# Optimization experiments

Measured on AMD Instinct MI355X. Metric: run time of the kernel, lower is better.

## Reference

```python
import jax, jax.numpy as jnp
import numpy as np

B, S, D, L = 4, 4096, 2048, 4
QH, KVH, WINDOW = 16, 4, 512
HD = D // QH
G = QH // KVH
CAPF = 0.25
EPS = float(jnp.finfo(jnp.float32).eps)  # torch RMSNorm default eps for fp32


def setup_inputs() -> dict:
    key = jax.random.key(0)
    ks = jax.random.split(key, 8)
    s = 0.02
    return {
        "x": jax.random.normal(ks[0], (B, S, D), jnp.float32),
        "router_w": jax.random.normal(ks[1], (1, D), jnp.float32) * s,
        "norm1_w": jnp.ones((L, D), jnp.float32),
        "norm2_w": jnp.ones((L, D), jnp.float32),
        "qkv_w": jax.random.normal(ks[2], (L, (QH + 2 * KVH) * HD, D), jnp.float32) * s,
        "proj_w": jax.random.normal(ks[3], (L, D, D), jnp.float32) * s,
        "fc1_w": jax.random.normal(ks[4], (L, 2 * D, D), jnp.float32) * s,
        "fc2_w": jax.random.normal(ks[5], (L, D, D), jnp.float32) * s,
    }


def rmsnorm(x, w):
    return x * jax.lax.rsqrt(jnp.mean(x * x, -1, keepdims=True) + EPS) * w


def gqa(x, qkv_w, proj_w):
    # x: [B, C, D]; causal sliding-window attention with ALiBi (flash_attn semantics)
    b, c, _ = x.shape
    qkv = x @ qkv_w.T
    q = qkv[..., : QH * HD].reshape(b, c, KVH, G, HD)
    k = qkv[..., QH * HD:(QH + KVH) * HD].reshape(b, c, KVH, HD)
    v = qkv[..., (QH + KVH) * HD:].reshape(b, c, KVH, HD)
    scale = 1.0 / np.sqrt(HD)
    scores = jnp.einsum('bqkgd,bskd->bkgqs', q, k) * scale  # [B,KVH,G,C,C]
    i = jnp.arange(c)[:, None]
    j = jnp.arange(c)[None, :]
    diff = (i - j).astype(jnp.float32)
    mask = (diff >= 0) & (diff <= WINDOW)  # causal + left window
    slopes = jnp.exp2(-((jnp.arange(QH, dtype=jnp.float32) + 1.0) * 8.0 / QH))
    slopes = slopes.reshape(KVH, G, 1, 1)  # q head h = kvh*G + g ordering
    scores = jnp.where(mask, scores - slopes * diff, -jnp.inf)
    p = jax.nn.softmax(scores, axis=-1)
    att = jnp.einsum('bkgqs,bskd->bqkgd', p, v).reshape(b, c, QH * HD)
    return att @ proj_w.T


def swiglu(x, fc1_w, fc2_w):
    h = x @ fc1_w.T
    a, gate = jnp.split(h, 2, axis=-1)
    return (jax.nn.silu(gate) * a) @ fc2_w.T


def reference(x, router_w, norm1_w, norm2_w, qkv_w, proj_w, fc1_w, fc2_w):
    b, s, d = x.shape
    rw = jax.nn.sigmoid(x @ router_w.T)  # [B, S, 1]
    cap = int(s * CAPF)  # training path: capacity = int(seq_len * capacity_factor)
    rws = rw[..., 0]
    _, top_idx = jax.lax.top_k(rws, cap)            # unsorted-by-position top-k
    idx_sorted = jnp.sort(top_idx, axis=1)          # restore sequence order
    order = jnp.argsort(top_idx, axis=1)
    # faithful to source: gathers router_weights at the sort-order permutation
    # indices (values in [0, cap)), exactly as torch.gather(router_weights, 1, router_top_order)
    top_w = jnp.take_along_axis(rws, order, axis=1)[..., None]  # [B, cap, 1]
    lat = jnp.take_along_axis(x, idx_sorted[..., None], axis=1)  # [B, cap, D]
    for l in range(L):
        lat = lat + gqa(rmsnorm(lat, norm1_w[l]), qkv_w[l], proj_w[l])
        lat = lat + swiglu(rmsnorm(lat, norm2_w[l]), fc1_w[l], fc2_w[l])
    lat = lat * top_w
    bidx = jnp.arange(b)[:, None]
    pred = jnp.zeros_like(x).at[bidx, idx_sorted].set(lat)
    decisions = jnp.zeros_like(rw).at[bidx, idx_sorted].set(1.0)
    return pred, rw, decisions
```

## Files before the change

### kernel.cpp

```cpp
#include <hip/hip_runtime.h>
#include <hip/hip_bf16.h>

constexpr int NB = 4;
constexpr int SEQ = 4096;
constexpr int DIM = 2048;
constexpr int NLAYER = 4;
constexpr int NQH = 16;
constexpr int NKVH = 4;
constexpr int WIN = 512;
constexpr int HDIM = 128;
constexpr int CAPN = 1024;
constexpr int MTOK = NB * CAPN;
constexpr int QKVN = (NQH + 2 * NKVH) * HDIM;
constexpr int VOFF = DIM + NKVH * HDIM;
constexpr float EPSF = 1.1920928955078125e-07f;

typedef __hip_bfloat16 bf16;
typedef __bf16 b16x8 __attribute__((ext_vector_type(8)));
typedef __bf16 b16x4 __attribute__((ext_vector_type(4)));
typedef float f32x4 __attribute__((ext_vector_type(4)));

#define MFMA16(a, b, c) __builtin_amdgcn_mfma_f32_16x16x32_bf16((a), (b), (c), 0, 0, 0)

__device__ __forceinline__ void gload_lds16(const void* g, void* l) {
  __builtin_amdgcn_global_load_lds((__attribute__((address_space(1))) void*)(void*)g,
                                   (__attribute__((address_space(3))) void*)l, 16, 0, 0);
}

__global__ __launch_bounds__(256) void cast_kernel(const float* __restrict__ in,
                                                   bf16* __restrict__ out, int n) {
  int i = (blockIdx.x * 256 + threadIdx.x) * 4;
  if (i >= n) return;
  float4 v = *(const float4*)(in + i);
  b16x4 o;
  o[0] = (__bf16)v.x; o[1] = (__bf16)v.y; o[2] = (__bf16)v.z; o[3] = (__bf16)v.w;
  *(b16x4*)((__bf16*)out + i) = o;
}

__global__ __launch_bounds__(256) void router_kernel(const float* __restrict__ x,
                                                     const float* __restrict__ rwt,
                                                     float* __restrict__ rw_out) {
  int tok = blockIdx.x * 4 + (threadIdx.x >> 6);
  int l = threadIdx.x & 63;
  const float* xr = x + (size_t)tok * DIM;
  float s = 0.f;
  for (int c = l; c < DIM; c += 64) s += xr[c] * rwt[c];
  for (int off = 32; off; off >>= 1) s += __shfl_down(s, off);
  if (l == 0) rw_out[tok] = 1.f / (1.f + expf(-s));
}

__global__ __launch_bounds__(256) void rankcnt_kernel(const float* __restrict__ rw,
                                                      int* __restrict__ rank) {
  int blk = blockIdx.x;
  int ic = blk & 15, jc = (blk >> 4) & 15, b = blk >> 8;
  __shared__ float4 svi[64];
  int t = threadIdx.x;
  if (t < 64) svi[t] = ((const float4*)(rw + (size_t)b * SEQ + ic * 256))[t];
  __syncthreads();
  int j = jc * 256 + t;
  float vj = rw[(size_t)b * SEQ + j];
  int r = 0;
#pragma unroll 16
  for (int q = 0; q < 64; ++q) {
    float4 v = svi[q];
    int i = ic * 256 + q * 4;
    r += (v.x > vj || (v.x == vj && (i + 0) < j)) ? 1 : 0;
    r += (v.y > vj || (v.y == vj && (i + 1) < j)) ? 1 : 0;
    r += (v.z > vj || (v.z == vj && (i + 2) < j)) ? 1 : 0;
    r += (v.w > vj || (v.w == vj && (i + 3) < j)) ? 1 : 0;
  }
  atomicAdd(&rank[b * SEQ + j], r);
}

__global__ __launch_bounds__(1024) void select_kernel(const int* __restrict__ rank,
                                                      const float* __restrict__ rw,
                                                      int* __restrict__ idxs,
                                                      float* __restrict__ topw,
                                                      float* __restrict__ dec) {
  int b = blockIdx.x;
  int t = threadIdx.x;
  __shared__ int sr[SEQ];
  __shared__ int scnt[1024];
  for (int i = t; i < SEQ; i += 1024) sr[i] = rank[b * SEQ + i];
  __syncthreads();
  for (int i = t; i < SEQ; i += 1024) dec[(size_t)b * SEQ + i] = (sr[i] < CAPN) ? 1.0f : 0.0f;
  int c = 0;
#pragma unroll
  for (int k = 0; k < 4; ++k) c += (sr[t * 4 + k] < CAPN) ? 1 : 0;
  scnt[t] = c;
  __syncthreads();
  for (int off = 1; off < 1024; off <<= 1) {
    int v = scnt[t];
    int vm = (t >= off) ? scnt[t - off] : 0;
    __syncthreads();
    scnt[t] = v + vm;
    __syncthreads();
  }
  int pos = scnt[t] - c;
  for (int k = 0; k < 4; ++k) {
    int j = t * 4 + k;
    int r = sr[j];
    if (r < CAPN) {
      idxs[b * CAPN + pos] = j;
      topw[b * CAPN + pos] = rw[(size_t)b * SEQ + r];
      pos++;
    }
  }
}

__global__ __launch_bounds__(256) void gather_kernel(const float* __restrict__ x,
                                                     const int* __restrict__ idxs,
                                                     float* __restrict__ lat) {
  int tok = blockIdx.x;
  int b = tok >> 10, i = tok & 1023;
  int src = idxs[b * CAPN + i];
  const float4* sp = (const float4*)(x + ((size_t)b * SEQ + src) * DIM);
  float4* dp = (float4*)(lat + (size_t)tok * DIM);
  int t = threadIdx.x;
  dp[t] = sp[t];
  dp[t + 256] = sp[t + 256];
}

__global__ __launch_bounds__(256) void rmsnorm_kernel(const float* __restrict__ in,
                                                      const float* __restrict__ w,
                                                      bf16* __restrict__ out) {
  int row = blockIdx.x;
  int t = threadIdx.x;
  const float4* sp = (const float4*)(in + (size_t)row * DIM);
  float4 v0 = sp[t], v1 = sp[t + 256];
  float ss = v0.x * v0.x + v0.y * v0.y + v0.z * v0.z + v0.w * v0.w +
             v1.x * v1.x + v1.y * v1.y + v1.z * v1.z + v1.w * v1.w;
  for (int off = 32; off; off >>= 1) ss += __shfl_down(ss, off);
  __shared__ float red[4];
  if ((t & 63) == 0) red[t >> 6] = ss;
  __syncthreads();
  float total = red[0] + red[1] + red[2] + red[3];
  float sc = rsqrtf(total * (1.0f / DIM) + EPSF);
  const float4* wp = (const float4*)w;
  float4 w0 = wp[t], w1 = wp[t + 256];
  __bf16* op = (__bf16*)out + (size_t)row * DIM;
  b16x4 o0, o1;
  o0[0] = (__bf16)(v0.x * w0.x * sc); o0[1] = (__bf16)(v0.y * w0.y * sc);
  o0[2] = (__bf16)(v0.z * w0.z * sc); o0[3] = (__bf16)(v0.w * w0.w * sc);
  o1[0] = (__bf16)(v1.x * w1.x * sc); o1[1] = (__bf16)(v1.y * w1.y * sc);
  o1[2] = (__bf16)(v1.z * w1.z * sc); o1[3] = (__bf16)(v1.w * w1.w * sc);
  *(b16x4*)(op + t * 4) = o0;
  *(b16x4*)(op + 1024 + t * 4) = o1;
}


__device__ __forceinline__ void stage_half(const bf16* g, int K, int kt,
                                           bf16* tilebase, int h, int tid) {
#pragma unroll
  for (int j = 0; j < 2; ++j) {
    int q = h * 16384 + j * 8192 + tid * 16;
    int row = q >> 7;
    int sc = ((tid & 7) ^ (row & 7)) << 3;
    gload_lds16((const __bf16*)g + (size_t)row * K + kt * 64 + sc,
                (char*)tilebase + q);
  }
}

__device__ __forceinline__ b16x8 frag8(const bf16* buf, int row, int ks, int hi) {
  int co = (ks * 32 + hi * 8) ^ ((row & 7) << 3);
  return *(const b16x8*)((const __bf16*)buf + row * 64 + co);
}

template <bool VT>
__global__ __launch_bounds__(512) void gemm8p(const bf16* __restrict__ A,
                                              const bf16* __restrict__ Bw,
                                              bf16* __restrict__ Cb,
                                              bf16* __restrict__ vTout,
                                              int N, int K, int nbn) {
  __shared__ __align__(16) bf16 sA[2][256 * 64];
  __shared__ __align__(16) bf16 sB[2][256 * 64];
  const int tid = threadIdx.x;
  const int w = tid >> 6, l = tid & 63;
  const int lo = l & 15, hi = l >> 4;
  const int wm = w >> 2, wn = w & 3;
  const int nwg = gridDim.x;
  int bid = blockIdx.x;
  bid = (bid & 7) * (nwg >> 3) + (bid >> 3);
  const int bm = bid / nbn, bn = bid % nbn;
  const bf16* Ab = A + (size_t)bm * 256 * K;
  const bf16* Bb = Bw + (size_t)bn * 256 * K;
  const int nt = K >> 6;
  const int niter = nt >> 1;

  f32x4 acc[8][4];
#pragma unroll
  for (int i = 0; i < 8; ++i)
#pragma unroll
    for (int j = 0; j < 4; ++j) acc[i][j] = f32x4{0.f, 0.f, 0.f, 0.f};

#define LDA_Q(BUF, QM)                                                      \
  do {                                                                      \
    _Pragma("unroll") for (int mi = 0; mi < 4; ++mi)                        \
        _Pragma("unroll") for (int ks = 0; ks < 2; ++ks)                    \
            af[mi][ks] = frag8((BUF), wm * 128 + (QM)*64 + mi * 16 + lo, ks, hi); \
  } while (0)
#define LDB_Q(BUF, QN, DST)                                                 \
  do {                                                                      \
    _Pragma("unroll") for (int ni = 0; ni < 2; ++ni)                        \
        _Pragma("unroll") for (int ks = 0; ks < 2; ++ks)                    \
            DST[ni][ks] = frag8((BUF), wn * 64 + (QN)*32 + ni * 16 + lo, ks, hi); \
  } while (0)
#define MM_Q(QM, QN, BFR)                                                   \
  do {                                                                      \
    __builtin_amdgcn_s_setprio(1);                                          \
    _Pragma("unroll") for (int ks = 0; ks < 2; ++ks)                        \
        _Pragma("unroll") for (int mi = 0; mi < 4; ++mi)                    \
            _Pragma("unroll") for (int ni = 0; ni < 2; ++ni)                \
                acc[(QM)*4 + mi][(QN)*2 + ni] =                             \
                    MFMA16(af[mi][ks], BFR[ni][ks], acc[(QM)*4 + mi][(QN)*2 + ni]); \
    __builtin_amdgcn_s_setprio(0);                                          \
  } while (0)
#define BAR() __builtin_amdgcn_s_barrier()

  stage_half(Ab, K, 0, sA[0], 0, tid);
  stage_half(Ab, K, 0, sA[0], 1, tid);
  stage_half(Bb, K, 0, sB[0], 0, tid);
  stage_half(Bb, K, 0, sB[0], 1, tid);
  stage_half(Bb, K, 1, sB[1], 0, tid);
  stage_half(Bb, K, 1, sB[1], 1, tid);
  stage_half(Ab, K, 1, sA[1], 0, tid);
  asm volatile("s_waitcnt vmcnt(6)" ::: "memory");
  __builtin_amdgcn_sched_barrier(0);
  BAR();

  for (int i = 0; i < niter; ++i) {
    const int t0 = 2 * i;
    const bool s2 = (t0 + 2) < nt;
    b16x8 af[4][2], bf0[2][2], bf1[2][2];
    LDA_Q(sA[0], 0); LDB_Q(sB[0], 0, bf0);
    stage_half(Ab, K, t0 + 1, sA[1], 1, tid);
    BAR(); MM_Q(0, 0, bf0); BAR();
    LDB_Q(sB[0], 1, bf1);
    BAR(); MM_Q(0, 1, bf1); BAR();
    LDA_Q(sA[0], 1);
    if (s2) stage_half(Bb, K, t0 + 2, sB[0], 0, tid);
    BAR(); MM_Q(1, 0, bf0); BAR();
    if (s2) stage_half(Bb, K, t0 + 2, sB[0], 1, tid);
    BAR(); MM_Q(1, 1, bf1);
    if (s2) asm volatile("s_waitcnt vmcnt(4)" ::: "memory");
    else    asm volatile("s_waitcnt vmcnt(0)" ::: "memory");
    __builtin_amdgcn_sched_barrier(0);
    BAR();
    LDA_Q(sA[1], 0); LDB_Q(sB[1], 0, bf0);
    if (s2) stage_half(Ab, K, t0 + 2, sA[0], 0, tid);
    BAR(); MM_Q(0, 0, bf0); BAR();
    LDB_Q(sB[1], 1, bf1);
    if (s2) stage_half(Ab, K, t0 + 2, sA[0], 1, tid);
    BAR(); MM_Q(0, 1, bf1); BAR();
    LDA_Q(sA[1], 1);
    if (s2) { stage_half(Bb, K, t0 + 3, sB[1], 0, tid);
              stage_half(Bb, K, t0 + 3, sB[1], 1, tid); }
    BAR(); MM_Q(1, 0, bf0); BAR();
    if (s2) stage_half(Ab, K, t0 + 3, sA[1], 0, tid);
    BAR(); MM_Q(1, 1, bf1);
    if (s2) {
      asm volatile("s_waitcnt vmcnt(6)" ::: "memory");
      __builtin_amdgcn_sched_barrier(0);
    }
    BAR();
  }
#undef LDA_Q
#undef LDB_Q
#undef MM_Q
#undef BAR

#pragma unroll
  for (int fi = 0; fi < 8; ++fi) {
    int row0 = bm * 256 + wm * 128 + fi * 16 + hi * 4;
#pragma unroll
    for (int fj = 0; fj < 4; ++fj) {
      int col = bn * 256 + wn * 64 + fj * 16 + lo;
#pragma unroll
      for (int r = 0; r < 4; ++r) {
        bf16 bv = __float2bfloat16(acc[fi][fj][r]);
        Cb[(size_t)(row0 + r) * N + col] = bv;
        if constexpr (VT) {
          if (col >= VOFF) {
            int cc = col - VOFF;
            int kvh = cc >> 7, d = cc & 127;
            int row = row0 + r;
            int bb = row >> 10, tk = row & 1023;
            vTout[((size_t)(bb * NKVH + kvh) * HDIM + d) * CAPN + tk] = bv;
          }
        }
      }
    }
  }
}

template <int ROWS>
__device__ __forceinline__ void stage_tile(const bf16* gbase, int ldk, int kt,
                                           bf16* lbuf, int tid) {
#pragma unroll
  for (int i = 0; i < ROWS / 128; ++i) {
    int q = i * 8192 + tid * 16;
    int row = q >> 6;
    int ce = ((tid & 3) ^ ((row >> 1) & 3)) << 3;
    gload_lds16((const __bf16*)gbase + (size_t)row * ldk + kt * 32 + ce,
                (char*)lbuf + q);
  }
}

__device__ __forceinline__ b16x8 frag_ld(const bf16* buf, int row, int hi) {
  int ce = (hi ^ ((row >> 1) & 3)) << 3;
  return *(const b16x8*)((const __bf16*)buf + row * 32 + ce);
}

template <int MR, bool ADD, bool OUTBF>
__global__ __launch_bounds__(512, 2) void gemm256(const bf16* __restrict__ A,
                                                  const bf16* __restrict__ Bw,
                                                  float* __restrict__ Cf,
                                                  bf16* __restrict__ Cb,
                                                  bf16* __restrict__ vTout,
                                                  int N, int K, int nbn) {
  constexpr int BM = MR * 32;
  constexpr int PH = MR / 4;
  __shared__ __align__(16) bf16 sA[4][BM * 32];
  __shared__ __align__(16) bf16 sB[4][256 * 32];
  const int tid = threadIdx.x;
  const int w = tid >> 6, l = tid & 63;
  const int lo = l & 15, hi = l >> 4;
  const int wm = w >> 2, wn = w & 3;
  const int nwg = gridDim.x;
  int bid = blockIdx.x;
  bid = (bid & 7) * (nwg >> 3) + (bid >> 3);
  const int bm = bid / nbn, bn = bid % nbn;
  const bf16* Ab = A + (size_t)bm * BM * K;
  const bf16* Bb = Bw + (size_t)bn * 256 * K;
  const int nt = K >> 5;

  f32x4 acc[MR][4];
#pragma unroll
  for (int i = 0; i < MR; ++i)
#pragma unroll
    for (int j = 0; j < 4; ++j) acc[i][j] = f32x4{0.f, 0.f, 0.f, 0.f};

  for (int tt = 0; tt < 3; ++tt) {
    stage_tile<BM>(Ab, K, tt, sA[tt], tid);
    stage_tile<256>(Bb, K, tt, sB[tt], tid);
  }
  if constexpr (MR == 8) asm volatile("s_waitcnt vmcnt(8)" ::: "memory");
  else                   asm volatile("s_waitcnt vmcnt(6)" ::: "memory");
  __builtin_amdgcn_sched_barrier(0);
  __builtin_amdgcn_s_barrier();

  for (int t = 0; t < nt; ++t) {
    const bf16* bufA = sA[t & 3];
    const bf16* bufB = sB[t & 3];
    b16x8 bfr[4];
#pragma unroll
    for (int p = 0; p < PH; ++p) {
      b16x8 af[4];
#pragma unroll
      for (int mi = 0; mi < 4; ++mi)
        af[mi] = frag_ld(bufA, wm * (MR * 16) + p * 64 + mi * 16 + lo, hi);
      if (p == 0) {
#pragma unroll
        for (int ni = 0; ni < 4; ++ni)
          bfr[ni] = frag_ld(bufB, wn * 64 + ni * 16 + lo, hi);
      }
      if (t + 3 < nt) {
        if (p == 0) stage_tile<BM>(Ab, K, t + 3, sA[(t + 3) & 3], tid);
        if (p == PH - 1) stage_tile<256>(Bb, K, t + 3, sB[(t + 3) & 3], tid);
      }
      __builtin_amdgcn_s_barrier();
      __builtin_amdgcn_s_setprio(1);
#pragma unroll
      for (int mi = 0; mi < 4; ++mi)
#pragma unroll
        for (int ni = 0; ni < 4; ++ni)
          acc[p * 4 + mi][ni] = MFMA16(af[mi], bfr[ni], acc[p * 4 + mi][ni]);
      __builtin_amdgcn_s_setprio(0);
      if (p == PH - 1) {
        if (t + 3 < nt) {
          if constexpr (MR == 8) asm volatile("s_waitcnt vmcnt(8)" ::: "memory");
          else                   asm volatile("s_waitcnt vmcnt(6)" ::: "memory");
        } else if (t + 2 < nt) {
          if constexpr (MR == 8) asm volatile("s_waitcnt vmcnt(4)" ::: "memory");
          else                   asm volatile("s_waitcnt vmcnt(3)" ::: "memory");
        } else if (t + 1 < nt) {
          asm volatile("s_waitcnt vmcnt(0)" ::: "memory");
        }
        __builtin_amdgcn_sched_barrier(0);
      }
      __builtin_amdgcn_s_barrier();
    }
  }

#pragma unroll
  for (int mi = 0; mi < MR; ++mi) {
    int row0 = bm * BM + wm * (MR * 16) + mi * 16 + hi * 4;
#pragma unroll
    for (int ni = 0; ni < 4; ++ni) {
      int col = bn * 256 + wn * 64 + ni * 16 + lo;
#pragma unroll
      for (int r = 0; r < 4; ++r) {
        size_t idx = (size_t)(row0 + r) * N + col;
        float v = acc[mi][ni][r];
        if constexpr (ADD) v += Cf[idx];
        if constexpr (OUTBF) {
          Cb[idx] = __float2bfloat16(v);
        } else {
          Cf[idx] = v;
        }
      }
    }
  }
}

__global__ __launch_bounds__(256) void attn_kernel(const bf16* __restrict__ qkvb,
                                                   const bf16* __restrict__ vT,
                                                   bf16* __restrict__ attb) {
  const int blk = blockIdx.x;
  const int qc = blk & 31;
  const int kvh = (blk >> 5) & 3;
  const int b = blk >> 7;
  const int w = threadIdx.x >> 6, l = threadIdx.x & 63;
  const int lo = l & 15, hi = l >> 4;
  const int h = kvh * 4 + w;
  const float slope = exp2f(-0.5f * (float)(h + 1));
  const float scale = 0.08838834764831845f;
  __shared__ __align__(16) bf16 p_lds[4][2][16 * 32];
  const __bf16* qp = (const __bf16*)qkvb;
  const __bf16* vtp = (const __bf16*)vT + (size_t)(b * NKVH + kvh) * HDIM * CAPN;
  const size_t tb = (size_t)b * CAPN;
  const int i0b = qc * 32;

  b16x8 aq[2][4];
#pragma unroll
  for (int qt = 0; qt < 2; ++qt) {
    const __bf16* qrow = qp + (tb + i0b + qt * 16 + lo) * QKVN + h * HDIM + hi * 8;
#pragma unroll
    for (int c = 0; c < 4; ++c) aq[qt][c] = *(const b16x8*)(qrow + c * 32);
  }

  f32x4 acc[2][8];
#pragma unroll
  for (int qt = 0; qt < 2; ++qt)
#pragma unroll
    for (int d = 0; d < 8; ++d) acc[qt][d] = f32x4{0.f, 0.f, 0.f, 0.f};
  float mrow[2][4], ssum[2][4];
#pragma unroll
  for (int qt = 0; qt < 2; ++qt)
#pragma unroll
    for (int r = 0; r < 4; ++r) { mrow[qt][r] = -1e30f; ssum[qt][r] = 0.f; }

  int jlo = i0b - WIN;
  if (jlo < 0) jlo = 0;
  jlo &= ~31;
  for (int j0 = jlo; j0 <= i0b; j0 += 32) {
    b16x8 kf[2][4];
#pragma unroll
    for (int jt = 0; jt < 2; ++jt) {
      const __bf16* krow = qp + (tb + j0 + jt * 16 + lo) * QKVN + DIM + kvh * HDIM + hi * 8;
#pragma unroll
      for (int c = 0; c < 4; ++c) kf[jt][c] = *(const b16x8*)(krow + c * 32);
    }
    f32x4 s[2][2];
#pragma unroll
    for (int qt = 0; qt < 2; ++qt)
#pragma unroll
      for (int jt = 0; jt < 2; ++jt) {
        s[qt][jt] = f32x4{0.f, 0.f, 0.f, 0.f};
#pragma unroll
        for (int c = 0; c < 4; ++c) s[qt][jt] = MFMA16(aq[qt][c], kf[jt][c], s[qt][jt]);
      }
#pragma unroll
    for (int qt = 0; qt < 2; ++qt) {
#pragma unroll
      for (int r = 0; r < 4; ++r) {
        const int i = i0b + qt * 16 + hi * 4 + r;
        float d0f = (float)(i - (j0 + lo));
        float d1f = (float)(i - (j0 + 16 + lo));
        float v0 = (d0f >= 0.f && d0f <= 512.f) ? (s[qt][0][r] * scale - slope * d0f) : -1e30f;
        float v1 = (d1f >= 0.f && d1f <= 512.f) ? (s[qt][1][r] * scale - slope * d1f) : -1e30f;
        float tm = fmaxf(v0, v1);
#pragma unroll
        for (int off = 1; off < 16; off <<= 1) tm = fmaxf(tm, __shfl_xor(tm, off));
        float mnew = fmaxf(mrow[qt][r], tm);
        float e0 = (v0 > -1e29f) ? __expf(v0 - mnew) : 0.f;
        float e1 = (v1 > -1e29f) ? __expf(v1 - mnew) : 0.f;
        float rs = e0 + e1;
#pragma unroll
        for (int off = 1; off < 16; off <<= 1) rs += __shfl_xor(rs, off);
        float corr = (mrow[qt][r] > -1e29f) ? __expf(mrow[qt][r] - mnew) : 0.f;
        ssum[qt][r] = ssum[qt][r] * corr + rs;
        mrow[qt][r] = mnew;
#pragma unroll
        for (int d = 0; d < 8; ++d) acc[qt][d][r] *= corr;
        p_lds[w][qt][(hi * 4 + r) * 32 + lo] = __float2bfloat16(e0);
        p_lds[w][qt][(hi * 4 + r) * 32 + 16 + lo] = __float2bfloat16(e1);
      }
    }
    b16x8 pa[2];
    pa[0] = *(const b16x8*)((const __bf16*)p_lds[w][0] + lo * 32 + hi * 8);
    pa[1] = *(const b16x8*)((const __bf16*)p_lds[w][1] + lo * 32 + hi * 8);
#pragma unroll
    for (int dh = 0; dh < 2; ++dh) {
      b16x8 bv[4];
#pragma unroll
      for (int dd = 0; dd < 4; ++dd) {
        int d = dh * 4 + dd;
        bv[dd] = *(const b16x8*)(vtp + (size_t)(d * 16 + lo) * CAPN + j0 + hi * 8);
      }
#pragma unroll
      for (int qt = 0; qt < 2; ++qt)
#pragma unroll
        for (int dd = 0; dd < 4; ++dd)
          acc[qt][dh * 4 + dd] = MFMA16(pa[qt], bv[dd], acc[qt][dh * 4 + dd]);
    }
  }
#pragma unroll
  for (int qt = 0; qt < 2; ++qt)
#pragma unroll
    for (int d = 0; d < 8; ++d)
#pragma unroll
      for (int r = 0; r < 4; ++r) {
        int row = i0b + qt * 16 + hi * 4 + r;
        attb[(tb + row) * DIM + h * HDIM + d * 16 + lo] =
            __float2bfloat16(acc[qt][d][r] / ssum[qt][r]);
      }
}

__global__ __launch_bounds__(256) void swiglu_kernel(const bf16* __restrict__ hb,
                                                     bf16* __restrict__ out) {
  int row = blockIdx.x;
  int c = threadIdx.x * 8;
  const __bf16* hp = (const __bf16*)hb + (size_t)row * (2 * DIM);
  b16x8 a8 = *(const b16x8*)(hp + c);
  b16x8 g8 = *(const b16x8*)(hp + DIM + c);
  b16x8 o;
#pragma unroll
  for (int i = 0; i < 8; ++i) {
    float a = (float)a8[i], g = (float)g8[i];
    float sg = g / (1.f + __expf(-g));
    o[i] = (__bf16)(sg * a);
  }
  *(b16x8*)((__bf16*)out + (size_t)row * DIM + c) = o;
}

__global__ __launch_bounds__(256) void scatter_kernel(const float* __restrict__ lat,
                                                      const int* __restrict__ idxs,
                                                      const float* __restrict__ topw,
                                                      float* __restrict__ pred) {
  int tok = blockIdx.x;
  int b = tok >> 10, i = tok & 1023;
  int dst = idxs[b * CAPN + i];
  float wv = topw[b * CAPN + i];
  const float4* sp = (const float4*)(lat + (size_t)tok * DIM);
  float4* dp = (float4*)(pred + ((size_t)b * SEQ + dst) * DIM);
  int t = threadIdx.x;
  float4 v = sp[t];
  v.x *= wv; v.y *= wv; v.z *= wv; v.w *= wv;
  dp[t] = v;
  v = sp[t + 256];
  v.x *= wv; v.y *= wv; v.z *= wv; v.w *= wv;
  dp[t + 256] = v;
}

extern "C" void kernel_launch(void* const* d_in, const int* in_sizes, int n_in,
                              void* d_out, int out_size, void* d_ws, size_t ws_size,
                              hipStream_t stream) {
  const float* x        = (const float*)d_in[0];
  const float* router_w = (const float*)d_in[1];
  const float* norm1_w  = (const float*)d_in[2];
  const float* norm2_w  = (const float*)d_in[3];
  const float* qkv_w    = (const float*)d_in[4];
  const float* proj_w   = (const float*)d_in[5];
  const float* fc1_w    = (const float*)d_in[6];
  const float* fc2_w    = (const float*)d_in[7];

  float* pred   = (float*)d_out;
  float* rw_out = pred + (size_t)NB * SEQ * DIM;
  float* dec    = rw_out + (size_t)NB * SEQ;

  char* ws = (char*)d_ws;
  float* lat  = (float*)ws; ws += (size_t)MTOK * DIM * 4;
  bf16* xn    = (bf16*)ws;  ws += (size_t)MTOK * DIM * 2;
  bf16* qkvb  = (bf16*)ws;  ws += (size_t)MTOK * QKVN * 2;
  bf16* attb  = (bf16*)ws;  ws += (size_t)MTOK * DIM * 2;
  int* rank   = (int*)ws;   ws += (size_t)NB * SEQ * 4;
  int* idxs   = (int*)ws;   ws += (size_t)NB * CAPN * 4;
  float* topw = (float*)ws; ws += (size_t)NB * CAPN * 4;

  char* sp = (char*)pred;
  bf16* hb = (bf16*)sp; sp += (size_t)MTOK * (2 * DIM) * 2;
  bf16* wq = (bf16*)sp; sp += (size_t)QKVN * DIM * 2;
  bf16* wp = (bf16*)sp; sp += (size_t)DIM * DIM * 2;
  bf16* w1 = (bf16*)sp; sp += (size_t)(2 * DIM) * DIM * 2;
  bf16* w2 = (bf16*)sp; sp += (size_t)DIM * DIM * 2;
  bf16* vT = (bf16*)sp; sp += (size_t)NB * NKVH * HDIM * CAPN * 2;

  router_kernel<<<NB * SEQ / 4, 256, 0, stream>>>(x, router_w, rw_out);
  hipMemsetAsync(rank, 0, (size_t)NB * SEQ * 4, stream);
  rankcnt_kernel<<<NB * 256, 256, 0, stream>>>(rw_out, rank);
  select_kernel<<<NB, 1024, 0, stream>>>(rank, rw_out, idxs, topw, dec);
  gather_kernel<<<MTOK, 256, 0, stream>>>(x, idxs, lat);

  for (int l = 0; l < NLAYER; ++l) {
    cast_kernel<<<(QKVN * DIM) / 1024, 256, 0, stream>>>(qkv_w + (size_t)l * QKVN * DIM, wq, QKVN * DIM);
    cast_kernel<<<(DIM * DIM) / 1024, 256, 0, stream>>>(proj_w + (size_t)l * DIM * DIM, wp, DIM * DIM);
    cast_kernel<<<(2 * DIM * DIM) / 1024, 256, 0, stream>>>(fc1_w + (size_t)l * 2 * DIM * DIM, w1, 2 * DIM * DIM);
    cast_kernel<<<(DIM * DIM) / 1024, 256, 0, stream>>>(fc2_w + (size_t)l * DIM * DIM, w2, DIM * DIM);

    rmsnorm_kernel<<<MTOK, 256, 0, stream>>>(lat, norm1_w + (size_t)l * DIM, xn);
    gemm8p<true><<<(MTOK / 256) * (QKVN / 256), 512, 0, stream>>>(
        xn, wq, qkvb, vT, QKVN, DIM, QKVN / 256);
    attn_kernel<<<NB * NKVH * 32, 256, 0, stream>>>(qkvb, vT, attb);
    gemm256<4, true, false><<<(MTOK / 128) * (DIM / 256), 512, 0, stream>>>(
        attb, wp, lat, nullptr, nullptr, DIM, DIM, DIM / 256);

    rmsnorm_kernel<<<MTOK, 256, 0, stream>>>(lat, norm2_w + (size_t)l * DIM, xn);
    gemm8p<false><<<(MTOK / 256) * (2 * DIM / 256), 512, 0, stream>>>(
        xn, w1, hb, nullptr, 2 * DIM, DIM, 2 * DIM / 256);
    swiglu_kernel<<<MTOK, 256, 0, stream>>>(hb, xn);
    gemm256<4, true, false><<<(MTOK / 128) * (DIM / 256), 512, 0, stream>>>(
        xn, w2, lat, nullptr, nullptr, DIM, DIM, DIM / 256);
  }

  hipMemsetAsync(pred, 0, (size_t)NB * SEQ * DIM * 4, stream);
  scatter_kernel<<<MTOK, 256, 0, stream>>>(lat, idxs, topw, pred);
}
```

Measured before the change: 1.675 ms.

## Fuse SwiGLU into fc1 GEMM epilogue via interleaved fc1 weight rows

The fc1 weight cast now interleaves the 'a' and 'gate' rows in 16-row chunks, so each 16-column MFMA fragment pair in the GEMM holds matching a/gate columns. The fc1 GEMM epilogue then applies silu(gate)*a directly and writes the DIM-wide bf16 activation, which removes the separate swiglu kernel and the round trip of the 2*DIM-wide intermediate through memory. The gemm8p staging schedule is also reordered so A tiles are issued as whole pairs with a changed vmcnt wait depth, and an unused vTout parameter is dropped from gemm256. The reordered prefetch could shift load/compute overlap in either direction.

```diff
diff --git a/kernel.cpp b/kernel.cpp
--- a/kernel.cpp
+++ b/kernel.cpp
@@ -35,6 +35,23 @@
   b16x4 o;
   o[0] = (__bf16)v.x; o[1] = (__bf16)v.y; o[2] = (__bf16)v.z; o[3] = (__bf16)v.w;
   *(b16x4*)((__bf16*)out + i) = o;
+}
+
+__global__ __launch_bounds__(256) void cast_fc1_kernel(const float* __restrict__ in,
+                                                       bf16* __restrict__ out) {
+  int p = blockIdx.x;
+  int chunk = p >> 5, w = p & 31;
+  int L = (w < 16) ? (chunk * 16 + w) : (DIM + chunk * 16 + (w - 16));
+  const float4* spv = (const float4*)(in + (size_t)L * DIM);
+  __bf16* op = (__bf16*)out + (size_t)p * DIM;
+  int t = threadIdx.x;
+#pragma unroll
+  for (int j = 0; j < 2; ++j) {
+    float4 v = spv[t + j * 256];
+    b16x4 o;
+    o[0] = (__bf16)v.x; o[1] = (__bf16)v.y; o[2] = (__bf16)v.z; o[3] = (__bf16)v.w;
+    *(b16x4*)(op + (t + j * 256) * 4) = o;
+  }
 }
 
 __global__ __launch_bounds__(256) void router_kernel(const float* __restrict__ x,
@@ -114,11 +131,11 @@
   int tok = blockIdx.x;
   int b = tok >> 10, i = tok & 1023;
   int src = idxs[b * CAPN + i];
-  const float4* sp = (const float4*)(x + ((size_t)b * SEQ + src) * DIM);
+  const float4* spv = (const float4*)(x + ((size_t)b * SEQ + src) * DIM);
   float4* dp = (float4*)(lat + (size_t)tok * DIM);
   int t = threadIdx.x;
-  dp[t] = sp[t];
-  dp[t + 256] = sp[t + 256];
+  dp[t] = spv[t];
+  dp[t + 256] = spv[t + 256];
 }
 
 __global__ __launch_bounds__(256) void rmsnorm_kernel(const float* __restrict__ in,
@@ -126,8 +143,8 @@
                                                       bf16* __restrict__ out) {
   int row = blockIdx.x;
   int t = threadIdx.x;
-  const float4* sp = (const float4*)(in + (size_t)row * DIM);
-  float4 v0 = sp[t], v1 = sp[t + 256];
+  const float4* spv = (const float4*)(in + (size_t)row * DIM);
+  float4 v0 = spv[t], v1 = spv[t + 256];
   float ss = v0.x * v0.x + v0.y * v0.y + v0.z * v0.z + v0.w * v0.w +
              v1.x * v1.x + v1.y * v1.y + v1.z * v1.z + v1.w * v1.w;
   for (int off = 32; off; off >>= 1) ss += __shfl_down(ss, off);
@@ -166,7 +183,7 @@
   return *(const b16x8*)((const __bf16*)buf + row * 64 + co);
 }
 
-template <bool VT>
+template <bool VT, bool SWI>
 __global__ __launch_bounds__(512) void gemm8p(const bf16* __restrict__ A,
                                               const bf16* __restrict__ Bw,
                                               bf16* __restrict__ Cb,
@@ -223,8 +240,7 @@
   stage_half(Bb, K, 0, sB[0], 1, tid);
   stage_half(Bb, K, 1, sB[1], 0, tid);
   stage_half(Bb, K, 1, sB[1], 1, tid);
-  stage_half(Ab, K, 1, sA[1], 0, tid);
-  asm volatile("s_waitcnt vmcnt(6)" ::: "memory");
+  asm volatile("s_waitcnt vmcnt(4)" ::: "memory");
   __builtin_amdgcn_sched_barrier(0);
   BAR();
 
@@ -233,33 +249,33 @@
     const bool s2 = (t0 + 2) < nt;
     b16x8 af[4][2], bf0[2][2], bf1[2][2];
     LDA_Q(sA[0], 0); LDB_Q(sB[0], 0, bf0);
+    stage_half(Ab, K, t0 + 1, sA[1], 0, tid);
     stage_half(Ab, K, t0 + 1, sA[1], 1, tid);
     BAR(); MM_Q(0, 0, bf0); BAR();
     LDB_Q(sB[0], 1, bf1);
     BAR(); MM_Q(0, 1, bf1); BAR();
     LDA_Q(sA[0], 1);
-    if (s2) stage_half(Bb, K, t0 + 2, sB[0], 0, tid);
     BAR(); MM_Q(1, 0, bf0); BAR();
-    if (s2) stage_half(Bb, K, t0 + 2, sB[0], 1, tid);
+    if (s2) { stage_half(Bb, K, t0 + 2, sB[0], 0, tid);
+              stage_half(Bb, K, t0 + 2, sB[0], 1, tid); }
     BAR(); MM_Q(1, 1, bf1);
     if (s2) asm volatile("s_waitcnt vmcnt(4)" ::: "memory");
     else    asm volatile("s_waitcnt vmcnt(0)" ::: "memory");
     __builtin_amdgcn_sched_barrier(0);
     BAR();
     LDA_Q(sA[1], 0); LDB_Q(sB[1], 0, bf0);
-    if (s2) stage_half(Ab, K, t0 + 2, sA[0], 0, tid);
+    if (s2) { stage_half(Ab, K, t0 + 2, sA[0], 0, tid);
+              stage_half(Ab, K, t0 + 2, sA[0], 1, tid); }
     BAR(); MM_Q(0, 0, bf0); BAR();
     LDB_Q(sB[1], 1, bf1);
-    if (s2) stage_half(Ab, K, t0 + 2, sA[0], 1, tid);
     BAR(); MM_Q(0, 1, bf1); BAR();
     LDA_Q(sA[1], 1);
+    BAR(); MM_Q(1, 0, bf0); BAR();
     if (s2) { stage_half(Bb, K, t0 + 3, sB[1], 0, tid);
               stage_half(Bb, K, t0 + 3, sB[1], 1, tid); }
-    BAR(); MM_Q(1, 0, bf0); BAR();
-    if (s2) stage_half(Ab, K, t0 + 3, sA[1], 0, tid);
     BAR(); MM_Q(1, 1, bf1);
     if (s2) {
-      asm volatile("s_waitcnt vmcnt(6)" ::: "memory");
+      asm volatile("s_waitcnt vmcnt(4)" ::: "memory");
       __builtin_amdgcn_sched_barrier(0);
     }
     BAR();
@@ -269,23 +285,41 @@
 #undef MM_Q
 #undef BAR
 
-#pragma unroll
-  for (int fi = 0; fi < 8; ++fi) {
-    int row0 = bm * 256 + wm * 128 + fi * 16 + hi * 4;
-#pragma unroll
-    for (int fj = 0; fj < 4; ++fj) {
-      int col = bn * 256 + wn * 64 + fj * 16 + lo;
-#pragma unroll
-      for (int r = 0; r < 4; ++r) {
-        bf16 bv = __float2bfloat16(acc[fi][fj][r]);
-        Cb[(size_t)(row0 + r) * N + col] = bv;
-        if constexpr (VT) {
-          if (col >= VOFF) {
-            int cc = col - VOFF;
-            int kvh = cc >> 7, d = cc & 127;
-            int row = row0 + r;
-            int bb = row >> 10, tk = row & 1023;
-            vTout[((size_t)(bb * NKVH + kvh) * HDIM + d) * CAPN + tk] = bv;
+  if constexpr (SWI) {
+#pragma unroll
+    for (int fi = 0; fi < 8; ++fi) {
+      int row0 = bm * 256 + wm * 128 + fi * 16 + hi * 4;
+#pragma unroll
+      for (int j2 = 0; j2 < 2; ++j2) {
+        int colL = bn * 128 + wn * 32 + j2 * 16 + lo;
+#pragma unroll
+        for (int r = 0; r < 4; ++r) {
+          float a = acc[fi][2 * j2][r];
+          float g = acc[fi][2 * j2 + 1][r];
+          float s = g / (1.f + __expf(-g));
+          Cb[(size_t)(row0 + r) * DIM + colL] = __float2bfloat16(a * s);
+        }
+      }
+    }
+  } else {
+#pragma unroll
+    for (int fi = 0; fi < 8; ++fi) {
+      int row0 = bm * 256 + wm * 128 + fi * 16 + hi * 4;
+#pragma unroll
+      for (int fj = 0; fj < 4; ++fj) {
+        int col = bn * 256 + wn * 64 + fj * 16 + lo;
+#pragma unroll
+        for (int r = 0; r < 4; ++r) {
+          bf16 bv = __float2bfloat16(acc[fi][fj][r]);
+          Cb[(size_t)(row0 + r) * N + col] = bv;
+          if constexpr (VT) {
+            if (col >= VOFF) {
+              int cc = col - VOFF;
+              int kvh = cc >> 7, d = cc & 127;
+              int row = row0 + r;
+              int bb = row >> 10, tk = row & 1023;
+              vTout[((size_t)(bb * NKVH + kvh) * HDIM + d) * CAPN + tk] = bv;
+            }
           }
         }
       }
@@ -316,7 +350,6 @@
                                                   const bf16* __restrict__ Bw,
                                                   float* __restrict__ Cf,
                                                   bf16* __restrict__ Cb,
-                                                  bf16* __restrict__ vTout,
                                                   int N, int K, int nbn) {
   constexpr int BM = MR * 32;
   constexpr int PH = MR / 4;
@@ -527,23 +560,6 @@
       }
 }
 
-__global__ __launch_bounds__(256) void swiglu_kernel(const bf16* __restrict__ hb,
-                                                     bf16* __restrict__ out) {
-  int row = blockIdx.x;
-  int c = threadIdx.x * 8;
-  const __bf16* hp = (const __bf16*)hb + (size_t)row * (2 * DIM);
-  b16x8 a8 = *(const b16x8*)(hp + c);
-  b16x8 g8 = *(const b16x8*)(hp + DIM + c);
-  b16x8 o;
-#pragma unroll
-  for (int i = 0; i < 8; ++i) {
-    float a = (float)a8[i], g = (float)g8[i];
-    float sg = g / (1.f + __expf(-g));
-    o[i] = (__bf16)(sg * a);
-  }
-  *(b16x8*)((__bf16*)out + (size_t)row * DIM + c) = o;
-}
-
 __global__ __launch_bounds__(256) void scatter_kernel(const float* __restrict__ lat,
                                                       const int* __restrict__ idxs,
                                                       const float* __restrict__ topw,
@@ -552,13 +568,13 @@
   int b = tok >> 10, i = tok & 1023;
   int dst = idxs[b * CAPN + i];
   float wv = topw[b * CAPN + i];
-  const float4* sp = (const float4*)(lat + (size_t)tok * DIM);
+  const float4* spv = (const float4*)(lat + (size_t)tok * DIM);
   float4* dp = (float4*)(pred + ((size_t)b * SEQ + dst) * DIM);
   int t = threadIdx.x;
-  float4 v = sp[t];
+  float4 v = spv[t];
   v.x *= wv; v.y *= wv; v.z *= wv; v.w *= wv;
   dp[t] = v;
-  v = sp[t + 256];
+  v = spv[t + 256];
   v.x *= wv; v.y *= wv; v.z *= wv; v.w *= wv;
   dp[t + 256] = v;
 }
@@ -589,7 +605,7 @@
   float* topw = (float*)ws; ws += (size_t)NB * CAPN * 4;
 
   char* sp = (char*)pred;
-  bf16* hb = (bf16*)sp; sp += (size_t)MTOK * (2 * DIM) * 2;
+  sp += (size_t)MTOK * (2 * DIM) * 2;
   bf16* wq = (bf16*)sp; sp += (size_t)QKVN * DIM * 2;
   bf16* wp = (bf16*)sp; sp += (size_t)DIM * DIM * 2;
   bf16* w1 = (bf16*)sp; sp += (size_t)(2 * DIM) * DIM * 2;
@@ -605,22 +621,21 @@
   for (int l = 0; l < NLAYER; ++l) {
     cast_kernel<<<(QKVN * DIM) / 1024, 256, 0, stream>>>(qkv_w + (size_t)l * QKVN * DIM, wq, QKVN * DIM);
     cast_kernel<<<(DIM * DIM) / 1024, 256, 0, stream>>>(proj_w + (size_t)l * DIM * DIM, wp, DIM * DIM);
-    cast_kernel<<<(2 * DIM * DIM) / 1024, 256, 0, stream>>>(fc1_w + (size_t)l * 2 * DIM * DIM, w1, 2 * DIM * DIM);
+    cast_fc1_kernel<<<2 * DIM, 256, 0, stream>>>(fc1_w + (size_t)l * 2 * DIM * DIM, w1);
     cast_kernel<<<(DIM * DIM) / 1024, 256, 0, stream>>>(fc2_w + (size_t)l * DIM * DIM, w2, DIM * DIM);
 
     rmsnorm_kernel<<<MTOK, 256, 0, stream>>>(lat, norm1_w + (size_t)l * DIM, xn);
-    gemm8p<true><<<(MTOK / 256) * (QKVN / 256), 512, 0, stream>>>(
+    gemm8p<true, false><<<(MTOK / 256) * (QKVN / 256), 512, 0, stream>>>(
         xn, wq, qkvb, vT, QKVN, DIM, QKVN / 256);
     attn_kernel<<<NB * NKVH * 32, 256, 0, stream>>>(qkvb, vT, attb);
     gemm256<4, true, false><<<(MTOK / 128) * (DIM / 256), 512, 0, stream>>>(
-        attb, wp, lat, nullptr, nullptr, DIM, DIM, DIM / 256);
+        attb, wp, lat, nullptr, DIM, DIM, DIM / 256);
 
     rmsnorm_kernel<<<MTOK, 256, 0, stream>>>(lat, norm2_w + (size_t)l * DIM, xn);
-    gemm8p<false><<<(MTOK / 256) * (2 * DIM / 256), 512, 0, stream>>>(
-        xn, w1, hb, nullptr, 2 * DIM, DIM, 2 * DIM / 256);
-    swiglu_kernel<<<MTOK, 256, 0, stream>>>(hb, xn);
+    gemm8p<false, true><<<(MTOK / 256) * (2 * DIM / 256), 512, 0, stream>>>(
+        xn, w1, attb, nullptr, 2 * DIM, DIM, 2 * DIM / 256);
     gemm256<4, true, false><<<(MTOK / 128) * (DIM / 256), 512, 0, stream>>>(
-        xn, w2, lat, nullptr, nullptr, DIM, DIM, DIM / 256);
+        attb, w2, lat, nullptr, DIM, DIM, DIM / 256);
   }
 
   hipMemsetAsync(pred, 0, (size_t)NB * SEQ * DIM * 4, stream);
```

Measured after the change: 1.613 ms. 1.04x faster.
